# Optimization experiments

Hardware: AMD Instinct MI355X
Metric: run time of the kernel (lower is better)

Reference implementation:

```python
import jax, jax.numpy as jnp
import numpy as np

B, L, D, T, V, H = 32, 48, 768, 32, 30522, 768

def build_iou_mask_map():
    # Faithful to the __init__ construction: banded validity mask [32, 33].
    m = np.zeros((32, 33), dtype=np.float32)
    for i in range(0, 32, 1):
        m[i, i + 1:min(i + 17, 33)] = 1.0
    for i in range(0, 32 - 16, 2):
        m[i, list(range(18 + i, 33, 2))] = 1.0
    return jnp.asarray(m)

def setup_inputs() -> dict:
    key = jax.random.key(0)
    ks = jax.random.split(key, 6)
    s = 0.02  # xavier-ish init scale
    return {
        'hidden_states_text': jax.random.normal(ks[0], (B, L, D), jnp.float32),
        'hidden_states_object': jax.random.normal(ks[1], (B, T + 1, D), jnp.float32),
        'w_t1': jax.random.normal(ks[2], (D, H), jnp.float32) * s,
        'b_t1': jnp.zeros((H,), jnp.float32),
        'w_t2': jax.random.normal(ks[3], (H, V), jnp.float32) * s,
        'b_t2': jnp.zeros((V,), jnp.float32),
        'w_i1': jax.random.normal(ks[4], (3 * D, H), jnp.float32) * s,
        'b_i1': jnp.zeros((H,), jnp.float32),
        'w_i2': jax.random.normal(ks[5], (H, 3), jnp.float32) * s,
        'b_i2': jnp.zeros((3,), jnp.float32),
    }

def reference(hidden_states_text, hidden_states_object,
              w_t1, b_t1, w_t2, b_t2, w_i1, b_i1, w_i2, b_i2):
    # final_mlp: Dropout(eval: id) -> Linear -> ReLU -> Dropout -> Linear
    logits_text = jax.nn.relu(hidden_states_text @ w_t1 + b_t1) @ w_t2 + b_t2  # [B,L,V]

    hc = hidden_states_object                # [B, T+1, D]
    t = hc.shape[1] - 1
    s_idx = jnp.arange(t)                    # [T]
    e_idx = jnp.arange(t + 1)                # [T+1]
    # (0.5*(s+e)).long() == floor division for non-negative ints
    c_idx = (s_idx[:, None] + e_idx[None, :]) // 2          # [T, T+1]
    c_point = hc[:, c_idx, :]                                # [B, T, T+1, D] gather
    d = hc.shape[-1]
    s_pts = jnp.broadcast_to(hc[:, :-1, None, :], (hc.shape[0], t, t + 1, d))
    e_pts = jnp.broadcast_to(hc[:, None, :, :], (hc.shape[0], t, t + 1, d))
    sce = jnp.concatenate([s_pts, c_point, e_pts], axis=-1)  # [B, T, T+1, 3D]

    # final_mlp_3: Linear(3D->H) -> ReLU -> Dropout(id) -> Linear(H->3)
    h = jax.nn.relu(jnp.einsum('bstf,fh->bsth', sce, w_i1) + b_i1)
    logits_iou = jnp.einsum('bsth,hk->bstk', h, w_i2) + b_i2  # [B,T,T+1,3]
    logits_iou = jnp.transpose(logits_iou, (0, 3, 1, 2))      # [B,3,T,T+1]

    return logits_text, logits_iou, build_iou_mask_map()
```

## Files before the change

kernel.cpp:

```cpp
#include <hip/hip_runtime.h>

typedef unsigned short u16;
typedef short v8s __attribute__((ext_vector_type(8)));
typedef float v4f __attribute__((ext_vector_type(4)));

#define KDIM 768
#define M_TEXT 1536
#define N_VOCAB 30522
#define N_VOCAB_PAD 30592
#define M_HC 1056
#define M_HC_PAD 1152
#define N_IOU 2304
#define OUT_IOU_OFF 46881792
#define OUT_MASK_OFF 46983168

__device__ __forceinline__ u16 f2bf(float f) {
  unsigned u = __float_as_uint(f);
  u += 0x7fffu + ((u >> 16) & 1u);
  return (u16)(u >> 16);
}

__global__ __launch_bounds__(256) void prep_cvt(const float* __restrict__ xt_in,
                                                const float* __restrict__ hc_in,
                                                u16* __restrict__ xt,
                                                u16* __restrict__ hcb) {
  const int NXT = M_TEXT * KDIM / 4;
  int i = blockIdx.x * 256 + threadIdx.x;
  if (i < NXT) {
    float4 v = ((const float4*)xt_in)[i];
    ushort4 o; o.x = f2bf(v.x); o.y = f2bf(v.y); o.z = f2bf(v.z); o.w = f2bf(v.w);
    ((ushort4*)xt)[i] = o;
  } else {
    int j = i - NXT;
    int row = j / 192;
    float4 v = make_float4(0.f, 0.f, 0.f, 0.f);
    if (row < M_HC) v = ((const float4*)hc_in)[j];
    ushort4 o; o.x = f2bf(v.x); o.y = f2bf(v.y); o.z = f2bf(v.z); o.w = f2bf(v.w);
    ((ushort4*)hcb)[j] = o;
  }
}

__global__ __launch_bounds__(256) void transpose_cvt(const float* __restrict__ in,
                                                     u16* __restrict__ out,
                                                     int C, long inBatch, long outBatch) {
  __shared__ float tile[64][65];
  const float* ip = in + (long)blockIdx.z * inBatch;
  u16* op = out + (long)blockIdx.z * outBatch;
  int r0 = blockIdx.x * 64, c0 = blockIdx.y * 64;
  int tx = threadIdx.x & 63, tg = threadIdx.x >> 6;
#pragma unroll
  for (int i = 0; i < 16; ++i) {
    int r = tg + i * 4;
    int gc = c0 + tx;
    tile[r][tx] = (gc < C) ? ip[(long)(r0 + r) * C + gc] : 0.f;
  }
  __syncthreads();
#pragma unroll
  for (int i = 0; i < 16; ++i) {
    int cc = tg + i * 4;
    op[(long)(c0 + cc) * KDIM + r0 + tx] = f2bf(tile[tx][cc]);
  }
}

__global__ void mask_kernel(float* __restrict__ out) {
  int idx = blockIdx.x * 256 + threadIdx.x;
  if (idx >= 1056) return;
  int i = idx / 33, j = idx % 33;
  float v = 0.f;
  int hi = min(i + 17, 33);
  if (j >= i + 1 && j < hi) v = 1.f;
  if ((i & 1) == 0 && i < 16 && j >= 18 + i && ((j - (18 + i)) & 1) == 0) v = 1.f;
  out[OUT_MASK_OFF + idx] = v;
}

template <int MODE>
__global__ __launch_bounds__(256)
void gemm_bt(const u16* __restrict__ A, const u16* __restrict__ BT,
             float* __restrict__ fout, u16* __restrict__ bfout,
             const float* __restrict__ bias, int ldc, int nmax) {
  __shared__ u16 sA[128 * 32];
  __shared__ u16 sB[128 * 32];
  const int tid = threadIdx.x;
  const int wid = tid >> 6;
  const int lane = tid & 63;
  const int lrow = lane & 15;
  const int quad = lane >> 4;
  const int wm = (wid & 1) * 64;
  const int wn = (wid >> 1) * 64;
  const int m0 = blockIdx.y * 128;
  const int n0 = blockIdx.x * 128;

  const int srow = wid * 32 + (lane >> 2);
  const int scol = (lane & 3) * 8;
  const u16* gA = A + (long)(m0 + srow) * KDIM + scol;
  const u16* gB = BT + (long)(n0 + srow) * KDIM + scol;
  u16* lA = &sA[(wid * 32) * 32];
  u16* lB = &sB[(wid * 32) * 32];

  v4f acc[4][4];
#pragma unroll
  for (int i = 0; i < 4; ++i)
#pragma unroll
    for (int j = 0; j < 4; ++j) acc[i][j] = (v4f){0.f, 0.f, 0.f, 0.f};

  const v8s* pA = (const v8s*)sA;
  const v8s* pB = (const v8s*)sB;
  const int ia0 = (wm + lrow) * 4 + quad;
  const int ib0 = (wn + lrow) * 4 + quad;

  for (int kt = 0; kt < KDIM / 32; ++kt) {
    const u16* ga = gA + kt * 32;
    const u16* gb = gB + kt * 32;
    __builtin_amdgcn_global_load_lds((const __attribute__((address_space(1))) void*)ga,
                                     (__attribute__((address_space(3))) void*)lA, 16, 0, 0);
    __builtin_amdgcn_global_load_lds((const __attribute__((address_space(1))) void*)(ga + 16 * KDIM),
                                     (__attribute__((address_space(3))) void*)(lA + 16 * 32), 16, 0, 0);
    __builtin_amdgcn_global_load_lds((const __attribute__((address_space(1))) void*)gb,
                                     (__attribute__((address_space(3))) void*)lB, 16, 0, 0);
    __builtin_amdgcn_global_load_lds((const __attribute__((address_space(1))) void*)(gb + 16 * KDIM),
                                     (__attribute__((address_space(3))) void*)(lB + 16 * 32), 16, 0, 0);
    __syncthreads();

    v8s af[4], bfr[4];
#pragma unroll
    for (int mt = 0; mt < 4; ++mt) af[mt] = pA[ia0 + mt * 64];
#pragma unroll
    for (int nt = 0; nt < 4; ++nt) bfr[nt] = pB[ib0 + nt * 64];
#pragma unroll
    for (int mt = 0; mt < 4; ++mt)
#pragma unroll
      for (int nt = 0; nt < 4; ++nt)
        acc[mt][nt] = __builtin_amdgcn_mfma_f32_16x16x32_bf16(af[mt], bfr[nt], acc[mt][nt], 0, 0, 0);
    __syncthreads();
  }

#pragma unroll
  for (int nt = 0; nt < 4; ++nt) {
    int c = n0 + wn + nt * 16 + lrow;
    float bv = 0.f;
    if (MODE == 0) { if (c < nmax) bv = bias[c]; }
    if (MODE == 1) bv = bias[c];
#pragma unroll
    for (int mt = 0; mt < 4; ++mt) {
#pragma unroll
      for (int r = 0; r < 4; ++r) {
        int row = m0 + wm + mt * 16 + quad * 4 + r;
        float v = acc[mt][nt][r] + bv;
        if (MODE == 0) {
          if (c < nmax) fout[(long)row * ldc + c] = v;
        } else if (MODE == 1) {
          bfout[(long)row * ldc + c] = f2bf(fmaxf(v, 0.f));
        } else {
          fout[(long)row * ldc + c] = v;
        }
      }
    }
  }
}

__global__ __launch_bounds__(256) void iou_combine(const float* __restrict__ Xcat,
                                                   const float* __restrict__ b1,
                                                   const float* __restrict__ w2,
                                                   const float* __restrict__ b2,
                                                   float* __restrict__ out) {
  int gw = (blockIdx.x * 256 + threadIdx.x) >> 6;
  int lane = threadIdx.x & 63;
  if (gw >= 32 * 32 * 33) return;
  int b = gw / 1056;
  int rem = gw % 1056;
  int s = rem / 33;
  int t = rem % 33;
  int cidx = (s + t) >> 1;
  const float* ps = Xcat + (long)(b * 33 + s) * N_IOU;
  const float* pc = Xcat + (long)(b * 33 + cidx) * N_IOU + 768;
  const float* pe = Xcat + (long)(b * 33 + t) * N_IOU + 1536;
  float a0 = 0.f, a1 = 0.f, a2 = 0.f;
#pragma unroll
  for (int j = 0; j < 3; ++j) {
    int h0 = j * 256 + lane * 4;
    float4 vs = *(const float4*)(ps + h0);
    float4 vc = *(const float4*)(pc + h0);
    float4 ve = *(const float4*)(pe + h0);
    float4 vb = *(const float4*)(b1 + h0);
    const float* fs = (const float*)&vs;
    const float* fc = (const float*)&vc;
    const float* fe = (const float*)&ve;
    const float* fb = (const float*)&vb;
#pragma unroll
    for (int c = 0; c < 4; ++c) {
      float v = fmaxf(fs[c] + fc[c] + fe[c] + fb[c], 0.f);
      int h = h0 + c;
      a0 += v * w2[h * 3 + 0];
      a1 += v * w2[h * 3 + 1];
      a2 += v * w2[h * 3 + 2];
    }
  }
#pragma unroll
  for (int off = 32; off > 0; off >>= 1) {
    a0 += __shfl_down(a0, off, 64);
    a1 += __shfl_down(a1, off, 64);
    a2 += __shfl_down(a2, off, 64);
  }
  if (lane == 0) {
    int base = OUT_IOU_OFF + b * 3168 + s * 33 + t;
    out[base + 0 * 1056] = a0 + b2[0];
    out[base + 1 * 1056] = a1 + b2[1];
    out[base + 2 * 1056] = a2 + b2[2];
  }
}

extern "C" void kernel_launch(void* const* d_in, const int* in_sizes, int n_in,
                              void* d_out, int out_size, void* d_ws, size_t ws_size,
                              hipStream_t stream) {
  const float* hst  = (const float*)d_in[0];
  const float* hso  = (const float*)d_in[1];
  const float* w_t1 = (const float*)d_in[2];
  const float* b_t1 = (const float*)d_in[3];
  const float* w_t2 = (const float*)d_in[4];
  const float* b_t2 = (const float*)d_in[5];
  const float* w_i1 = (const float*)d_in[6];
  const float* b_i1 = (const float*)d_in[7];
  const float* w_i2 = (const float*)d_in[8];
  const float* b_i2 = (const float*)d_in[9];
  float* out = (float*)d_out;

  char* ws = (char*)d_ws;
  u16*   w_t2T = (u16*)(ws + 0);
  u16*   xt    = (u16*)(ws + 46989312);
  u16*   w_t1T = (u16*)(ws + 49348608);
  u16*   htext = (u16*)(ws + 50528256);
  u16*   hcb   = (u16*)(ws + 52887552);
  u16*   w_i1T = (u16*)(ws + 54657024);
  float* Xcat  = (float*)(ws + 58195968);

  prep_cvt<<<dim3(2016), dim3(256), 0, stream>>>(hst, hso, xt, hcb);
  transpose_cvt<<<dim3(12, 12, 1), dim3(256), 0, stream>>>(w_t1, w_t1T, 768, 0, 0);
  transpose_cvt<<<dim3(12, N_VOCAB_PAD / 64, 1), dim3(256), 0, stream>>>(w_t2, w_t2T, N_VOCAB, 0, 0);
  transpose_cvt<<<dim3(12, 12, 3), dim3(256), 0, stream>>>(w_i1, w_i1T, 768, 768L * 768, 768L * 768);
  mask_kernel<<<dim3(5), dim3(256), 0, stream>>>(out);

  gemm_bt<1><<<dim3(KDIM / 128, M_TEXT / 128), dim3(256), 0, stream>>>(
      xt, w_t1T, nullptr, htext, b_t1, KDIM, KDIM);
  gemm_bt<0><<<dim3(N_VOCAB_PAD / 128, M_TEXT / 128), dim3(256), 0, stream>>>(
      htext, w_t2T, out, nullptr, b_t2, N_VOCAB, N_VOCAB);

  gemm_bt<2><<<dim3(N_IOU / 128, M_HC_PAD / 128), dim3(256), 0, stream>>>(
      hcb, w_i1T, Xcat, nullptr, nullptr, N_IOU, N_IOU);
  iou_combine<<<dim3(8448), dim3(256), 0, stream>>>(Xcat, b_i1, w_i2, b_i2, out);
}
```

Measured before the change: 527.5 us.

## Use 256x128 vocab GEMM tile with LDS-staged coalesced output stores

Adds a dedicated vocab-projection GEMM that uses 256-row tiles. This doubles the per-wave M work and reuses each B tile across more rows. The epilogue stages accumulators through shared memory so that rows of the N_VOCAB-strided fp32 logits are written coalesced with the bias add. It also folds the mask fill into the prep kernel to drop one launch, and vectorises the w_i2 loads in iou_combine. The larger tile raises register pressure (128 accumulator floats per lane) and halves the grid rows, which may cut occupancy.

```diff
diff --git a/kernel.cpp b/kernel.cpp
--- a/kernel.cpp
+++ b/kernel.cpp
@@ -23,20 +23,32 @@
 __global__ __launch_bounds__(256) void prep_cvt(const float* __restrict__ xt_in,
                                                 const float* __restrict__ hc_in,
                                                 u16* __restrict__ xt,
-                                                u16* __restrict__ hcb) {
+                                                u16* __restrict__ hcb,
+                                                float* __restrict__ out) {
   const int NXT = M_TEXT * KDIM / 4;
+  const int NHC = 1152 * 192;
   int i = blockIdx.x * 256 + threadIdx.x;
   if (i < NXT) {
     float4 v = ((const float4*)xt_in)[i];
     ushort4 o; o.x = f2bf(v.x); o.y = f2bf(v.y); o.z = f2bf(v.z); o.w = f2bf(v.w);
     ((ushort4*)xt)[i] = o;
-  } else {
+  } else if (i < NXT + NHC) {
     int j = i - NXT;
     int row = j / 192;
     float4 v = make_float4(0.f, 0.f, 0.f, 0.f);
     if (row < M_HC) v = ((const float4*)hc_in)[j];
     ushort4 o; o.x = f2bf(v.x); o.y = f2bf(v.y); o.z = f2bf(v.z); o.w = f2bf(v.w);
     ((ushort4*)hcb)[j] = o;
+  } else {
+    int idx = i - (NXT + NHC);
+    if (idx < 1056) {
+      int r = idx / 33, c = idx % 33;
+      float v = 0.f;
+      int hi = min(r + 17, 33);
+      if (c >= r + 1 && c < hi) v = 1.f;
+      if ((r & 1) == 0 && r < 16 && c >= 18 + r && ((c - (18 + r)) & 1) == 0) v = 1.f;
+      out[OUT_MASK_OFF + idx] = v;
+    }
   }
 }
 
@@ -62,22 +74,11 @@
   }
 }
 
-__global__ void mask_kernel(float* __restrict__ out) {
-  int idx = blockIdx.x * 256 + threadIdx.x;
-  if (idx >= 1056) return;
-  int i = idx / 33, j = idx % 33;
-  float v = 0.f;
-  int hi = min(i + 17, 33);
-  if (j >= i + 1 && j < hi) v = 1.f;
-  if ((i & 1) == 0 && i < 16 && j >= 18 + i && ((j - (18 + i)) & 1) == 0) v = 1.f;
-  out[OUT_MASK_OFF + idx] = v;
-}
-
 template <int MODE>
 __global__ __launch_bounds__(256)
 void gemm_bt(const u16* __restrict__ A, const u16* __restrict__ BT,
              float* __restrict__ fout, u16* __restrict__ bfout,
-             const float* __restrict__ bias, int ldc, int nmax) {
+             const float* __restrict__ bias, int ldc) {
   __shared__ u16 sA[128 * 32];
   __shared__ u16 sB[128 * 32];
   const int tid = threadIdx.x;
@@ -137,23 +138,107 @@
 #pragma unroll
   for (int nt = 0; nt < 4; ++nt) {
     int c = n0 + wn + nt * 16 + lrow;
-    float bv = 0.f;
-    if (MODE == 0) { if (c < nmax) bv = bias[c]; }
-    if (MODE == 1) bv = bias[c];
+    float bv = (MODE == 1) ? bias[c] : 0.f;
 #pragma unroll
     for (int mt = 0; mt < 4; ++mt) {
 #pragma unroll
       for (int r = 0; r < 4; ++r) {
         int row = m0 + wm + mt * 16 + quad * 4 + r;
         float v = acc[mt][nt][r] + bv;
-        if (MODE == 0) {
-          if (c < nmax) fout[(long)row * ldc + c] = v;
-        } else if (MODE == 1) {
+        if (MODE == 1) {
           bfout[(long)row * ldc + c] = f2bf(fmaxf(v, 0.f));
         } else {
           fout[(long)row * ldc + c] = v;
         }
       }
+    }
+  }
+}
+
+__global__ __launch_bounds__(256)
+void gemm_bt_v(const u16* __restrict__ A, const u16* __restrict__ BT,
+               float* __restrict__ fout, const float* __restrict__ bias) {
+  __shared__ char smem[64 * 132 * 4];
+  u16* sA = (u16*)smem;
+  u16* sB = (u16*)(smem + 16384);
+  float* sC = (float*)smem;
+
+  const int tid = threadIdx.x;
+  const int wid = tid >> 6;
+  const int lane = tid & 63;
+  const int lrow = lane & 15;
+  const int quad = lane >> 4;
+  const int wm = (wid & 1) * 128;
+  const int wn = (wid >> 1) * 64;
+  const int m0 = blockIdx.y * 256;
+  const int n0 = blockIdx.x * 128;
+
+  const int lr = lane >> 2;
+  const int lc = (lane & 3) * 8;
+  const u16* gA = A + (long)(m0 + wid * 64 + lr) * KDIM + lc;
+  const u16* gB = BT + (long)(n0 + wid * 32 + lr) * KDIM + lc;
+  u16* lA = sA + (wid * 64) * 32;
+  u16* lB = sB + (wid * 32) * 32;
+
+  v4f acc[8][4];
+#pragma unroll
+  for (int i = 0; i < 8; ++i)
+#pragma unroll
+    for (int j = 0; j < 4; ++j) acc[i][j] = (v4f){0.f, 0.f, 0.f, 0.f};
+
+  const v8s* pA = (const v8s*)sA;
+  const v8s* pB = (const v8s*)sB;
+  const int ia0 = (wm + lrow) * 4 + quad;
+  const int ib0 = (wn + lrow) * 4 + quad;
+
+  for (int kt = 0; kt < KDIM / 32; ++kt) {
+    const u16* ga = gA + kt * 32;
+    const u16* gb = gB + kt * 32;
+#pragma unroll
+    for (int j = 0; j < 4; ++j)
+      __builtin_amdgcn_global_load_lds((const __attribute__((address_space(1))) void*)(ga + j * 16 * KDIM),
+                                       (__attribute__((address_space(3))) void*)(lA + j * 16 * 32), 16, 0, 0);
+#pragma unroll
+    for (int j = 0; j < 2; ++j)
+      __builtin_amdgcn_global_load_lds((const __attribute__((address_space(1))) void*)(gb + j * 16 * KDIM),
+                                       (__attribute__((address_space(3))) void*)(lB + j * 16 * 32), 16, 0, 0);
+    __syncthreads();
+
+    v8s af[8], bfr[4];
+#pragma unroll
+    for (int mt = 0; mt < 8; ++mt) af[mt] = pA[ia0 + mt * 64];
+#pragma unroll
+    for (int nt = 0; nt < 4; ++nt) bfr[nt] = pB[ib0 + nt * 64];
+#pragma unroll
+    for (int mt = 0; mt < 8; ++mt)
+#pragma unroll
+      for (int nt = 0; nt < 4; ++nt)
+        acc[mt][nt] = __builtin_amdgcn_mfma_f32_16x16x32_bf16(af[mt], bfr[nt], acc[mt][nt], 0, 0, 0);
+    __syncthreads();
+  }
+
+#pragma unroll
+  for (int p = 0; p < 4; ++p) {
+    __syncthreads();
+    if ((wid & 1) == (p >> 1)) {
+      const int mtb = (p & 1) * 4;
+#pragma unroll
+      for (int mt2 = 0; mt2 < 4; ++mt2)
+#pragma unroll
+        for (int nt = 0; nt < 4; ++nt)
+#pragma unroll
+          for (int r = 0; r < 4; ++r)
+            sC[(mt2 * 16 + quad * 4 + r) * 132 + wn + nt * 16 + lrow] = acc[mtb + mt2][nt][r];
+    }
+    __syncthreads();
+    const int rbase = m0 + p * 64;
+#pragma unroll
+    for (int j = 0; j < 32; ++j) {
+      int flat = j * 256 + tid;
+      int rw = flat >> 7, cl = flat & 127;
+      int c = n0 + cl;
+      if (c < N_VOCAB)
+        fout[(long)(rbase + rw) * N_VOCAB + c] = sC[rw * 132 + cl] + bias[c];
     }
   }
 }
@@ -182,17 +267,21 @@
     float4 vc = *(const float4*)(pc + h0);
     float4 ve = *(const float4*)(pe + h0);
     float4 vb = *(const float4*)(b1 + h0);
+    float4 w0 = *(const float4*)(w2 + h0 * 3);
+    float4 w1 = *(const float4*)(w2 + h0 * 3 + 4);
+    float4 wv2 = *(const float4*)(w2 + h0 * 3 + 8);
     const float* fs = (const float*)&vs;
     const float* fc = (const float*)&vc;
     const float* fe = (const float*)&ve;
     const float* fb = (const float*)&vb;
+    float wf[12];
+    *(float4*)&wf[0] = w0; *(float4*)&wf[4] = w1; *(float4*)&wf[8] = wv2;
 #pragma unroll
     for (int c = 0; c < 4; ++c) {
       float v = fmaxf(fs[c] + fc[c] + fe[c] + fb[c], 0.f);
-      int h = h0 + c;
-      a0 += v * w2[h * 3 + 0];
-      a1 += v * w2[h * 3 + 1];
-      a2 += v * w2[h * 3 + 2];
+      a0 += v * wf[c * 3 + 0];
+      a1 += v * wf[c * 3 + 1];
+      a2 += v * wf[c * 3 + 2];
     }
   }
 #pragma unroll
@@ -233,18 +322,17 @@
   u16*   w_i1T = (u16*)(ws + 54657024);
   float* Xcat  = (float*)(ws + 58195968);
 
-  prep_cvt<<<dim3(2016), dim3(256), 0, stream>>>(hst, hso, xt, hcb);
+  prep_cvt<<<dim3(2021), dim3(256), 0, stream>>>(hst, hso, xt, hcb, out);
   transpose_cvt<<<dim3(12, 12, 1), dim3(256), 0, stream>>>(w_t1, w_t1T, 768, 0, 0);
   transpose_cvt<<<dim3(12, N_VOCAB_PAD / 64, 1), dim3(256), 0, stream>>>(w_t2, w_t2T, N_VOCAB, 0, 0);
   transpose_cvt<<<dim3(12, 12, 3), dim3(256), 0, stream>>>(w_i1, w_i1T, 768, 768L * 768, 768L * 768);
-  mask_kernel<<<dim3(5), dim3(256), 0, stream>>>(out);
 
   gemm_bt<1><<<dim3(KDIM / 128, M_TEXT / 128), dim3(256), 0, stream>>>(
-      xt, w_t1T, nullptr, htext, b_t1, KDIM, KDIM);
-  gemm_bt<0><<<dim3(N_VOCAB_PAD / 128, M_TEXT / 128), dim3(256), 0, stream>>>(
-      htext, w_t2T, out, nullptr, b_t2, N_VOCAB, N_VOCAB);
+      xt, w_t1T, nullptr, htext, b_t1, KDIM);
+  gemm_bt_v<<<dim3(N_VOCAB_PAD / 128, M_TEXT / 256), dim3(256), 0, stream>>>(
+      htext, w_t2T, out, b_t2);
 
   gemm_bt<2><<<dim3(N_IOU / 128, M_HC_PAD / 128), dim3(256), 0, stream>>>(
-      hcb, w_i1T, Xcat, nullptr, nullptr, N_IOU, N_IOU);
+      hcb, w_i1T, Xcat, nullptr, nullptr, N_IOU);
   iou_combine<<<dim3(8448), dim3(256), 0, stream>>>(Xcat, b_i1, w_i2, b_i2, out);
 }
```

Result: slower. 548.1 us (+3.9%).
